# Kernel optimization log

Hardware: AMD Instinct MI355X
Metric: run time of the kernel (lower is better)

## Reference

```python
import jax, jax.numpy as jnp
import numpy as np

M_POOL = 12500  # rows of the down_transform sparse matrix


def setup_inputs() -> dict:
    key = jax.random.key(0)
    ks = jax.random.split(key, 6)
    B, N, E, Cin, Cout, K, P = 4, 50000, 800000, 32, 64, 6, 50000
    x = jax.random.normal(ks[0], (B, N, Cin), jnp.float32)
    edge_index = jax.random.randint(ks[1], (2, E), 0, N, dtype=jnp.int64)
    pool_row = jax.random.randint(ks[2], (P,), 0, M_POOL, dtype=jnp.int64)
    pool_col = jax.random.randint(ks[3], (P,), 0, N, dtype=jnp.int64)
    pool_val = jax.random.uniform(ks[4], (P,), jnp.float32)
    # xavier_uniform over each [Cin, Cout] slice; bias zero-init (reset_parameters)
    limit = np.sqrt(6.0 / (Cin + Cout)).astype(np.float32)
    weight = jax.random.uniform(ks[5], (K, Cin, Cout), jnp.float32, -limit, limit)
    bias = jnp.zeros((Cout,), jnp.float32)
    return dict(x=x, edge_index=edge_index, pool_row=pool_row,
                pool_col=pool_col, pool_val=pool_val, weight=weight, bias=bias)


def _cheb_conv(x, edge_index, weight, bias):
    # x: [B, N, Cin]; weight: [K, Cin, Cout]
    N = x.shape[1]
    row, col = edge_index[0], edge_index[1]
    ones = jnp.ones(row.shape, x.dtype)
    deg = jax.ops.segment_sum(ones, row, num_segments=N)
    dis = jnp.where(deg > 0, jax.lax.rsqrt(jnp.where(deg > 0, deg, 1.0)), 0.0)
    # L_hat = 2L/lambda_max - I with lambda_max=2, sym norm -> diag 0, off-diag -d_i^-1/2 d_j^-1/2
    norm = -dis[row] * dis[col]  # [E]

    def prop(h):  # h: [B, N, C] -> L_hat @ h (gather, scale, scatter_add)
        msgs = h[:, col, :] * norm[None, :, None]  # [B, E, C]
        return jnp.zeros_like(h).at[:, row, :].add(msgs)

    Tx0 = x
    out = jnp.einsum('bnc,co->bno', Tx0, weight[0])
    Tx1 = prop(Tx0)
    out = out + jnp.einsum('bnc,co->bno', Tx1, weight[1])
    for k in range(2, weight.shape[0]):
        Tx2 = 2.0 * prop(Tx1) - Tx0
        out = out + jnp.einsum('bnc,co->bno', Tx2, weight[k])
        Tx0, Tx1 = Tx1, Tx2
    return out + bias


def reference(x, edge_index, pool_row, pool_col, pool_val, weight, bias):
    h = _cheb_conv(x, edge_index, weight, bias)  # single block (n_blocks=1)
    h = jax.nn.elu(h)
    # Pool: gather columns, scale by sparse values, scatter_add into rows
    B, _, C = h.shape
    gathered = h[:, pool_col, :] * pool_val[None, :, None]  # [B, P, C]
    out = jnp.zeros((B, M_POOL, C), h.dtype).at[:, pool_row, :].add(gathered)
    return out
```

## Files before the change

### kernel.cpp

```cpp
#include <hip/hip_runtime.h>
#include <hip/hip_fp16.h>
#include <cstdint>

#define N_NODES 50000
#define B_SZ 4
#define C_IN 32
#define C_OUT 64
#define K_CHEB 6
#define M_POOL 12500
#define NT_ROWS (N_NODES + M_POOL)
#define NS32 ((size_t)N_NODES * C_IN)
#define ZH ((size_t)N_NODES * C_OUT)
#define CN_CAP 2048
#define DSTR 16

typedef _Float16 f16x8 __attribute__((ext_vector_type(8)));
typedef float f32x4 __attribute__((ext_vector_type(4)));
typedef unsigned short ushort_t;

__device__ __forceinline__ unsigned short f2h(float f) {
    union { _Float16 h; unsigned short u; } v;
    v.h = (_Float16)f;
    return v.u;
}

__device__ __forceinline__ float h2f(unsigned short u) {
    union { unsigned short u; _Float16 h; } v;
    v.u = u;
    return (float)v.h;
}

__device__ __forceinline__ __half2 u2h2(unsigned u) { return __builtin_bit_cast(__half2, u); }
__device__ __forceinline__ unsigned h22u(__half2 h) { return __builtin_bit_cast(unsigned, h); }

__global__ void zero_deg_kernel(int* __restrict__ deg_s) {
    int i = blockIdx.x * 256 + threadIdx.x;
    if (i < NT_ROWS * DSTR) deg_s[i] = 0;
}

__global__ void deg_slot_kernel(const int* __restrict__ row, const int* __restrict__ prow,
                                int* __restrict__ deg_s, int* __restrict__ slot, int E, int P) {
    int e = blockIdx.x * blockDim.x + threadIdx.x;
    if (e < E) slot[e] = atomicAdd(&deg_s[row[e] * DSTR], 1);
    else if (e < E + P) slot[e] = atomicAdd(&deg_s[(N_NODES + prow[e - E]) * DSTR], 1);
}

__global__ void disdegp_kernel(const int* __restrict__ deg_s, float* __restrict__ dis,
                               int* __restrict__ degp) {
    int i = blockIdx.x * blockDim.x + threadIdx.x;
    if (i < N_NODES) {
        int d = deg_s[i * DSTR];
        dis[i] = d > 0 ? rsqrtf((float)d) : 0.f;
        degp[i] = (d + 7) & ~7;
    } else if (i < NT_ROWS) {
        degp[i] = deg_s[i * DSTR];
    }
}

__global__ void block_sum_kernel(const int* __restrict__ degp, int* __restrict__ bsum, int N) {
    __shared__ int sm[256];
    int i = blockIdx.x * 256 + threadIdx.x;
    sm[threadIdx.x] = (i < N) ? degp[i] : 0;
    __syncthreads();
    for (int s = 128; s > 0; s >>= 1) {
        if (threadIdx.x < s) sm[threadIdx.x] += sm[threadIdx.x + s];
        __syncthreads();
    }
    if (threadIdx.x == 0) bsum[blockIdx.x] = sm[0];
}

__global__ void scan_bsum_kernel(int* bsum, int nb, int* rowptr, int N) {
    __shared__ int sm[256];
    int t = threadIdx.x;
    int v = (t < nb) ? bsum[t] : 0;
    sm[t] = v;
    __syncthreads();
    for (int off = 1; off < 256; off <<= 1) {
        int u = (t >= off) ? sm[t - off] : 0;
        __syncthreads();
        sm[t] += u;
        __syncthreads();
    }
    if (t < nb) bsum[t] = sm[t] - v;
    if (t == 0) rowptr[N] = sm[255];
}

__global__ void rowptr_kernel(const int* __restrict__ degp, const int* __restrict__ bsum,
                              int* __restrict__ rowptr, int N) {
    __shared__ int sm[256];
    int i = blockIdx.x * 256 + threadIdx.x;
    sm[threadIdx.x] = (i < N) ? degp[i] : 0;
    __syncthreads();
    if (threadIdx.x == 0) {
        int run = bsum[blockIdx.x];
        for (int t = 0; t < 256; t++) { int v = sm[t]; sm[t] = run; run += v; }
    }
    __syncthreads();
    if (i < N) rowptr[i] = sm[threadIdx.x];
}

__global__ void pad_fill_kernel(const int* __restrict__ deg_s, const int* __restrict__ rowptr,
                                int2* __restrict__ cn) {
    int r = blockIdx.x * blockDim.x + threadIdx.x;
    if (r >= N_NODES) return;
    int p = rowptr[r] + deg_s[r * DSTR];
    int p1 = rowptr[r + 1];
    for (; p < p1; ++p) cn[p] = make_int2(0, 0);
}

__global__ void place_all_kernel(const int* __restrict__ row, const int* __restrict__ col,
                                 const int* __restrict__ prow, const int* __restrict__ pcol,
                                 const float* __restrict__ pval, const float* __restrict__ dis,
                                 const int* __restrict__ rowptr, const int* __restrict__ slot,
                                 int2* __restrict__ cn, int E, int P) {
    int e = blockIdx.x * blockDim.x + threadIdx.x;
    if (e < E) {
        int r = row[e], c = col[e];
        float nm = -dis[r] * dis[c];
        unsigned h = f2h(nm);
        cn[rowptr[r] + slot[e]] = make_int2(c, (int)(h | (h << 16)));
    } else if (e < E + P) {
        int i = e - E;
        int r = N_NODES + prow[i];
        cn[rowptr[r] + slot[e]] = make_int2(pcol[i], __float_as_int(pval[i]));
    }
}

__global__ void cast_h_kernel(const float* __restrict__ in, unsigned int* __restrict__ out,
                              int n2) {
    int i = blockIdx.x * 256 + threadIdx.x;
    if (i < n2) {
        unsigned a = f2h(in[2 * i]), b = f2h(in[2 * i + 1]);
        out[i] = a | (b << 16);
    }
}

__global__ void __launch_bounds__(256, 8)
prop_kernel(const ushort_t* __restrict__ hf, const ushort_t* __restrict__ p2f,
            ushort_t* __restrict__ outf,
            const int* __restrict__ rowptr, const int2* __restrict__ cn, float alpha) {
    __shared__ int2 lcn[CN_CAP];
    int bid = blockIdx.x;
    int b = bid & 3;
    int grp = bid >> 2;
    int r0 = grp * 64;
    int rend = r0 + 64 > N_NODES ? N_NODES : r0 + 64;
    int pbase = rowptr[r0];
    int pend = rowptr[rend];
    int cnt = pend - pbase;
    bool use_lds = (cnt <= CN_CAP);
    if (use_lds) {
        for (int i = threadIdx.x; i < cnt; i += 256) lcn[i] = cn[pbase + i];
    }
    __syncthreads();

    int lr = threadIdx.x >> 2;
    int cs = threadIdx.x & 3;
    int r = r0 + lr;
    if (r >= N_NODES) return;
    const char* hb = (const char*)hf + (size_t)b * NS32 * 2;
    unsigned coff = (unsigned)cs * 16u;
    __half2 a0 = __float2half2_rn(0.f), a1 = a0, a2 = a0, a3 = a0;

    if (use_lds) {
        int p0 = rowptr[r] - pbase, p1 = rowptr[r + 1] - pbase;
        for (int p = p0; p < p1; p += 8) {
            unsigned off[8];
            __half2 n[8];
#pragma unroll
            for (int i = 0; i < 8; i++) {
                int2 e = lcn[p + i];
                off[i] = ((unsigned)e.x << 6) + coff;
                n[i] = u2h2((unsigned)e.y);
            }
            uint4 v[8];
#pragma unroll
            for (int i = 0; i < 8; i++) v[i] = *(const uint4*)(hb + off[i]);
#pragma unroll
            for (int i = 0; i < 8; i++) {
                a0 = __hfma2(u2h2(v[i].x), n[i], a0);
                a1 = __hfma2(u2h2(v[i].y), n[i], a1);
                a2 = __hfma2(u2h2(v[i].z), n[i], a2);
                a3 = __hfma2(u2h2(v[i].w), n[i], a3);
            }
        }
    } else {
        int p0 = rowptr[r], p1 = rowptr[r + 1];
        for (int p = p0; p < p1; p += 8) {
            unsigned off[8];
            __half2 n[8];
#pragma unroll
            for (int i = 0; i < 8; i++) {
                int2 e = cn[p + i];
                off[i] = ((unsigned)e.x << 6) + coff;
                n[i] = u2h2((unsigned)e.y);
            }
            uint4 v[8];
#pragma unroll
            for (int i = 0; i < 8; i++) v[i] = *(const uint4*)(hb + off[i]);
#pragma unroll
            for (int i = 0; i < 8; i++) {
                a0 = __hfma2(u2h2(v[i].x), n[i], a0);
                a1 = __hfma2(u2h2(v[i].y), n[i], a1);
                a2 = __hfma2(u2h2(v[i].z), n[i], a2);
                a3 = __hfma2(u2h2(v[i].w), n[i], a3);
            }
        }
    }

    unsigned ooff = ((unsigned)r << 6) + coff;
    uint4 o;
    if (p2f) {
        __half2 al2 = __float2half2_rn(alpha);
        uint4 pv = *(const uint4*)((const char*)p2f + (size_t)b * NS32 * 2 + ooff);
        o.x = h22u(__hfma2(a0, al2, __hneg2(u2h2(pv.x))));
        o.y = h22u(__hfma2(a1, al2, __hneg2(u2h2(pv.y))));
        o.z = h22u(__hfma2(a2, al2, __hneg2(u2h2(pv.z))));
        o.w = h22u(__hfma2(a3, al2, __hneg2(u2h2(pv.w))));
    } else {
        o.x = h22u(a0); o.y = h22u(a1); o.z = h22u(a2); o.w = h22u(a3);
    }
    *(uint4*)((char*)outf + (size_t)b * NS32 * 2 + ooff) = o;
}

__global__ void packW_kernel(const float* __restrict__ W, ushort_t* __restrict__ Wp) {
    int i = blockIdx.x * 256 + threadIdx.x;
    if (i >= K_CHEB * 4 * 64 * 8) return;
    int j = i & 7;
    int lane = (i >> 3) & 63;
    int t = (i >> 9) & 3;
    int s = i >> 11;
    int k = (lane >> 4) * 8 + j;
    int col = t * 16 + (lane & 15);
    Wp[i] = f2h(W[((size_t)s * C_IN + k) * C_OUT + col]);
}

__global__ void gemm_mfma_kernel(const ushort_t* __restrict__ T0, const ushort_t* __restrict__ T1,
                                 const ushort_t* __restrict__ T2, const ushort_t* __restrict__ T3,
                                 const ushort_t* __restrict__ T4, const ushort_t* __restrict__ T5,
                                 const ushort_t* __restrict__ Wp,
                                 const float* __restrict__ bias, ushort_t* __restrict__ z) {
    int lane = threadIdx.x & 63;
    int wave = (blockIdx.x << 2) + (threadIdx.x >> 6);
    int r0 = wave << 4;
    int ga = r0 + (lane & 15);
    int koff = (lane >> 4) * 8;
    const ushort_t* Ts[6] = {T0, T1, T2, T3, T4, T5};

    f16x8 afr[6];
#pragma unroll
    for (int s = 0; s < 6; s++)
        afr[s] = *(const f16x8*)(Ts[s] + (size_t)ga * C_IN + koff);

    int orow = r0 + ((lane >> 4) << 2);
#pragma unroll
    for (int t = 0; t < 4; t++) {
        f32x4 acc = {0.f, 0.f, 0.f, 0.f};
#pragma unroll
        for (int s = 0; s < 6; s++) {
            f16x8 bfr = *(const f16x8*)(Wp + ((s * 4 + t) * 64 + lane) * 8);
            acc = __builtin_amdgcn_mfma_f32_16x16x32_f16(afr[s], bfr, acc, 0, 0, 0);
        }
        int col = (t << 4) + (lane & 15);
        float bv = bias[col];
#pragma unroll
        for (int rg = 0; rg < 4; rg++) {
            float v = acc[rg] + bv;
            z[(size_t)(orow + rg) * C_OUT + col] = f2h(v > 0.f ? v : (expf(v) - 1.f));
        }
    }
}

__global__ void pool_csr_kernel(const ushort_t* __restrict__ z, const int* __restrict__ rowptr,
                                const int2* __restrict__ cn, float* __restrict__ out) {
    int bid = blockIdx.x;
    int b = bid & 3;
    int r = (bid >> 2) * 8 + (threadIdx.x >> 5);
    int c2 = threadIdx.x & 31;
    if (r >= M_POOL) return;
    const char* zb = (const char*)z + (size_t)b * ZH * 2;
    unsigned coff = (unsigned)c2 << 2;
    float s0 = 0.f, s1 = 0.f;
    int p0 = rowptr[N_NODES + r], p1 = rowptr[N_NODES + r + 1];
    for (int p = p0; p < p1; ++p) {
        int2 e = cn[p];
        float v = __int_as_float(e.y);
        unsigned u = *(const unsigned*)(zb + (((unsigned)e.x << 7) + coff));
        s0 += h2f((ushort_t)u) * v;
        s1 += h2f((ushort_t)(u >> 16)) * v;
    }
    size_t idx = (size_t)b * M_POOL * C_OUT + (size_t)r * C_OUT + 2 * c2;
    *(float2*)&out[idx] = make_float2(s0, s1);
}

extern "C" void kernel_launch(void* const* d_in, const int* in_sizes, int n_in,
                              void* d_out, int out_size, void* d_ws, size_t ws_size,
                              hipStream_t stream) {
    const float* x    = (const float*)d_in[0];
    const int*   ei   = (const int*)d_in[1];
    const int*   prow = (const int*)d_in[2];
    const int*   pcol = (const int*)d_in[3];
    const float* pval = (const float*)d_in[4];
    const float* W    = (const float*)d_in[5];
    const float* bias = (const float*)d_in[6];
    const int E = in_sizes[1] / 2;
    const int P = in_sizes[2];
    const int* row = ei;
    const int* col = ei + E;
    const int EP_MAX = E + 7 * N_NODES + P;

    char* ws = (char*)d_ws;
    size_t o = 0;
    auto alloc = [&](size_t bytes) -> char* {
        char* p = ws + o;
        o += (bytes + 255) & ~(size_t)255;
        return p;
    };
    int nb = (NT_ROWS + 255) / 256;
    int*   deg_s  = (int*)alloc((size_t)NT_ROWS * DSTR * 4);
    int*   degp   = (int*)alloc((size_t)NT_ROWS * 4);
    float* dis    = (float*)alloc((size_t)N_NODES * 4);
    int*   rowptr = (int*)alloc((size_t)(NT_ROWS + 1) * 4);
    int*   slot   = (int*)alloc((size_t)(E + P) * 4);
    int*   bsum   = (int*)alloc((size_t)nb * 4);
    int2*  cn     = (int2*)alloc((size_t)EP_MAX * 8);
    ushort_t* Wp  = (ushort_t*)alloc((size_t)K_CHEB * 4 * 64 * 8 * 2);
    ushort_t* xh  = (ushort_t*)alloc((size_t)B_SZ * NS32 * 2);
    ushort_t* hA  = (ushort_t*)alloc((size_t)B_SZ * NS32 * 2);
    ushort_t* hB  = (ushort_t*)alloc((size_t)B_SZ * NS32 * 2);
    ushort_t* hC  = (ushort_t*)alloc((size_t)B_SZ * NS32 * 2);
    ushort_t* hD  = (ushort_t*)alloc((size_t)B_SZ * NS32 * 2);
    ushort_t* hE  = (ushort_t*)alloc((size_t)B_SZ * NS32 * 2);
    ushort_t* z   = (ushort_t*)alloc((size_t)B_SZ * ZH * 2);

    zero_deg_kernel<<<(NT_ROWS * DSTR + 255) / 256, 256, 0, stream>>>(deg_s);
    deg_slot_kernel<<<(E + P + 255) / 256, 256, 0, stream>>>(row, prow, deg_s, slot, E, P);
    disdegp_kernel<<<nb, 256, 0, stream>>>(deg_s, dis, degp);
    block_sum_kernel<<<nb, 256, 0, stream>>>(degp, bsum, NT_ROWS);
    scan_bsum_kernel<<<1, 256, 0, stream>>>(bsum, nb, rowptr, NT_ROWS);
    rowptr_kernel<<<nb, 256, 0, stream>>>(degp, bsum, rowptr, NT_ROWS);
    pad_fill_kernel<<<(N_NODES + 255) / 256, 256, 0, stream>>>(deg_s, rowptr, cn);
    place_all_kernel<<<(E + P + 255) / 256, 256, 0, stream>>>(row, col, prow, pcol, pval, dis,
                                                              rowptr, slot, cn, E, P);
    packW_kernel<<<(K_CHEB * 4 * 64 * 8 + 255) / 256, 256, 0, stream>>>(W, Wp);
    int n2 = (int)(B_SZ * NS32 / 2);
    cast_h_kernel<<<(n2 + 255) / 256, 256, 0, stream>>>(x, (unsigned int*)xh, n2);

    int prop_blocks = ((N_NODES + 63) / 64) * B_SZ;
    int gemm_blocks = (B_SZ * N_NODES) / 64;

    prop_kernel<<<prop_blocks, 256, 0, stream>>>(xh, nullptr, hA, rowptr, cn, 1.0f);
    prop_kernel<<<prop_blocks, 256, 0, stream>>>(hA, xh, hB, rowptr, cn, 2.0f);
    prop_kernel<<<prop_blocks, 256, 0, stream>>>(hB, hA, hC, rowptr, cn, 2.0f);
    prop_kernel<<<prop_blocks, 256, 0, stream>>>(hC, hB, hD, rowptr, cn, 2.0f);
    prop_kernel<<<prop_blocks, 256, 0, stream>>>(hD, hC, hE, rowptr, cn, 2.0f);
    gemm_mfma_kernel<<<gemm_blocks, 256, 0, stream>>>(xh, hA, hB, hC, hD, hE, Wp, bias, z);
    pool_csr_kernel<<<((M_POOL + 7) / 8) * B_SZ, 256, 0, stream>>>(z, rowptr, cn,
                                                                   (float*)d_out);
}
```

Before: 253.6 us.

## Fuse setup kernels, parallelize rowptr scan, add nontemporal loads/stores

```diff
diff --git a/kernel.cpp b/kernel.cpp
--- a/kernel.cpp
+++ b/kernel.cpp
@@ -13,9 +13,11 @@
 #define ZH ((size_t)N_NODES * C_OUT)
 #define CN_CAP 2048
 #define DSTR 16
+#define NWELEM (K_CHEB * 4 * 64 * 8)
 
 typedef _Float16 f16x8 __attribute__((ext_vector_type(8)));
 typedef float f32x4 __attribute__((ext_vector_type(4)));
+typedef unsigned int u32x4 __attribute__((ext_vector_type(4)));
 typedef unsigned short ushort_t;
 
 __device__ __forceinline__ unsigned short f2h(float f) {
@@ -45,22 +47,21 @@
     else if (e < E + P) slot[e] = atomicAdd(&deg_s[(N_NODES + prow[e - E]) * DSTR], 1);
 }
 
-__global__ void disdegp_kernel(const int* __restrict__ deg_s, float* __restrict__ dis,
-                               int* __restrict__ degp) {
-    int i = blockIdx.x * blockDim.x + threadIdx.x;
+__global__ void disdegp_bsum_kernel(const int* __restrict__ deg_s, float* __restrict__ dis,
+                                    int* __restrict__ degp, int* __restrict__ bsum) {
+    __shared__ int sm[256];
+    int i = blockIdx.x * 256 + threadIdx.x;
+    int dp = 0;
     if (i < N_NODES) {
         int d = deg_s[i * DSTR];
         dis[i] = d > 0 ? rsqrtf((float)d) : 0.f;
-        degp[i] = (d + 7) & ~7;
+        dp = (d + 7) & ~7;
+        degp[i] = dp;
     } else if (i < NT_ROWS) {
-        degp[i] = deg_s[i * DSTR];
-    }
-}
-
-__global__ void block_sum_kernel(const int* __restrict__ degp, int* __restrict__ bsum, int N) {
-    __shared__ int sm[256];
-    int i = blockIdx.x * 256 + threadIdx.x;
-    sm[threadIdx.x] = (i < N) ? degp[i] : 0;
+        dp = deg_s[i * DSTR];
+        degp[i] = dp;
+    }
+    sm[threadIdx.x] = dp;
     __syncthreads();
     for (int s = 128; s > 0; s >>= 1) {
         if (threadIdx.x < s) sm[threadIdx.x] += sm[threadIdx.x + s];
@@ -89,29 +90,24 @@
                               int* __restrict__ rowptr, int N) {
     __shared__ int sm[256];
     int i = blockIdx.x * 256 + threadIdx.x;
-    sm[threadIdx.x] = (i < N) ? degp[i] : 0;
+    int t = threadIdx.x;
+    int v = (i < N) ? degp[i] : 0;
+    sm[t] = v;
     __syncthreads();
-    if (threadIdx.x == 0) {
-        int run = bsum[blockIdx.x];
-        for (int t = 0; t < 256; t++) { int v = sm[t]; sm[t] = run; run += v; }
-    }
-    __syncthreads();
-    if (i < N) rowptr[i] = sm[threadIdx.x];
-}
-
-__global__ void pad_fill_kernel(const int* __restrict__ deg_s, const int* __restrict__ rowptr,
-                                int2* __restrict__ cn) {
-    int r = blockIdx.x * blockDim.x + threadIdx.x;
-    if (r >= N_NODES) return;
-    int p = rowptr[r] + deg_s[r * DSTR];
-    int p1 = rowptr[r + 1];
-    for (; p < p1; ++p) cn[p] = make_int2(0, 0);
-}
-
-__global__ void place_all_kernel(const int* __restrict__ row, const int* __restrict__ col,
+    for (int off = 1; off < 256; off <<= 1) {
+        int u = (t >= off) ? sm[t - off] : 0;
+        __syncthreads();
+        sm[t] += u;
+        __syncthreads();
+    }
+    if (i < N) rowptr[i] = bsum[blockIdx.x] + sm[t] - v;
+}
+
+__global__ void place_pad_kernel(const int* __restrict__ row, const int* __restrict__ col,
                                  const int* __restrict__ prow, const int* __restrict__ pcol,
                                  const float* __restrict__ pval, const float* __restrict__ dis,
                                  const int* __restrict__ rowptr, const int* __restrict__ slot,
+                                 const int* __restrict__ deg_s,
                                  int2* __restrict__ cn, int E, int P) {
     int e = blockIdx.x * blockDim.x + threadIdx.x;
     if (e < E) {
@@ -123,15 +119,32 @@
         int i = e - E;
         int r = N_NODES + prow[i];
         cn[rowptr[r] + slot[e]] = make_int2(pcol[i], __float_as_int(pval[i]));
-    }
-}
-
-__global__ void cast_h_kernel(const float* __restrict__ in, unsigned int* __restrict__ out,
-                              int n2) {
+    } else if (e < E + P + N_NODES) {
+        int r = e - E - P;
+        int p = rowptr[r] + deg_s[r * DSTR];
+        int p1 = rowptr[r + 1];
+        for (; p < p1; ++p) cn[p] = make_int2(0, 0);
+    }
+}
+
+__global__ void packW_cast_kernel(const float* __restrict__ W, ushort_t* __restrict__ Wp,
+                                  const float* __restrict__ xin, unsigned int* __restrict__ xout,
+                                  int n2) {
     int i = blockIdx.x * 256 + threadIdx.x;
-    if (i < n2) {
-        unsigned a = f2h(in[2 * i]), b = f2h(in[2 * i + 1]);
-        out[i] = a | (b << 16);
+    if (i < NWELEM) {
+        int j = i & 7;
+        int lane = (i >> 3) & 63;
+        int t = (i >> 9) & 3;
+        int s = i >> 11;
+        int k = (lane >> 4) * 8 + j;
+        int colw = t * 16 + (lane & 15);
+        Wp[i] = f2h(W[((size_t)s * C_IN + k) * C_OUT + colw]);
+    } else {
+        int c = i - NWELEM;
+        if (c < n2) {
+            unsigned a = f2h(xin[2 * c]), b = f2h(xin[2 * c + 1]);
+            xout[c] = a | (b << 16);
+        }
     }
 }
 
@@ -150,7 +163,11 @@
     int cnt = pend - pbase;
     bool use_lds = (cnt <= CN_CAP);
     if (use_lds) {
-        for (int i = threadIdx.x; i < cnt; i += 256) lcn[i] = cn[pbase + i];
+        for (int i = threadIdx.x; i < cnt; i += 256) {
+            unsigned long long u =
+                __builtin_nontemporal_load((const unsigned long long*)(cn + pbase + i));
+            lcn[i] = make_int2((int)(unsigned)(u & 0xffffffffULL), (int)(unsigned)(u >> 32));
+        }
     }
     __syncthreads();
 
@@ -209,30 +226,19 @@
     }
 
     unsigned ooff = ((unsigned)r << 6) + coff;
-    uint4 o;
+    u32x4 o;
     if (p2f) {
         __half2 al2 = __float2half2_rn(alpha);
-        uint4 pv = *(const uint4*)((const char*)p2f + (size_t)b * NS32 * 2 + ooff);
-        o.x = h22u(__hfma2(a0, al2, __hneg2(u2h2(pv.x))));
-        o.y = h22u(__hfma2(a1, al2, __hneg2(u2h2(pv.y))));
-        o.z = h22u(__hfma2(a2, al2, __hneg2(u2h2(pv.z))));
-        o.w = h22u(__hfma2(a3, al2, __hneg2(u2h2(pv.w))));
+        u32x4 pv = __builtin_nontemporal_load(
+            (const u32x4*)((const char*)p2f + (size_t)b * NS32 * 2 + ooff));
+        o[0] = h22u(__hfma2(a0, al2, __hneg2(u2h2(pv[0]))));
+        o[1] = h22u(__hfma2(a1, al2, __hneg2(u2h2(pv[1]))));
+        o[2] = h22u(__hfma2(a2, al2, __hneg2(u2h2(pv[2]))));
+        o[3] = h22u(__hfma2(a3, al2, __hneg2(u2h2(pv[3]))));
     } else {
-        o.x = h22u(a0); o.y = h22u(a1); o.z = h22u(a2); o.w = h22u(a3);
-    }
-    *(uint4*)((char*)outf + (size_t)b * NS32 * 2 + ooff) = o;
-}
-
-__global__ void packW_kernel(const float* __restrict__ W, ushort_t* __restrict__ Wp) {
-    int i = blockIdx.x * 256 + threadIdx.x;
-    if (i >= K_CHEB * 4 * 64 * 8) return;
-    int j = i & 7;
-    int lane = (i >> 3) & 63;
-    int t = (i >> 9) & 3;
-    int s = i >> 11;
-    int k = (lane >> 4) * 8 + j;
-    int col = t * 16 + (lane & 15);
-    Wp[i] = f2h(W[((size_t)s * C_IN + k) * C_OUT + col]);
+        o[0] = h22u(a0); o[1] = h22u(a1); o[2] = h22u(a2); o[3] = h22u(a3);
+    }
+    __builtin_nontemporal_store(o, (u32x4*)((char*)outf + (size_t)b * NS32 * 2 + ooff));
 }
 
 __global__ void gemm_mfma_kernel(const ushort_t* __restrict__ T0, const ushort_t* __restrict__ T1,
@@ -283,9 +289,11 @@
     float s0 = 0.f, s1 = 0.f;
     int p0 = rowptr[N_NODES + r], p1 = rowptr[N_NODES + r + 1];
     for (int p = p0; p < p1; ++p) {
-        int2 e = cn[p];
-        float v = __int_as_float(e.y);
-        unsigned u = *(const unsigned*)(zb + (((unsigned)e.x << 7) + coff));
+        unsigned long long eu =
+            __builtin_nontemporal_load((const unsigned long long*)(cn + p));
+        unsigned ex = (unsigned)(eu & 0xffffffffULL);
+        float v = __uint_as_float((unsigned)(eu >> 32));
+        unsigned u = *(const unsigned*)(zb + ((ex << 7) + coff));
         s0 += h2f((ushort_t)u) * v;
         s1 += h2f((ushort_t)(u >> 16)) * v;
     }
@@ -324,7 +332,7 @@
     int*   slot   = (int*)alloc((size_t)(E + P) * 4);
     int*   bsum   = (int*)alloc((size_t)nb * 4);
     int2*  cn     = (int2*)alloc((size_t)EP_MAX * 8);
-    ushort_t* Wp  = (ushort_t*)alloc((size_t)K_CHEB * 4 * 64 * 8 * 2);
+    ushort_t* Wp  = (ushort_t*)alloc((size_t)NWELEM * 2);
     ushort_t* xh  = (ushort_t*)alloc((size_t)B_SZ * NS32 * 2);
     ushort_t* hA  = (ushort_t*)alloc((size_t)B_SZ * NS32 * 2);
     ushort_t* hB  = (ushort_t*)alloc((size_t)B_SZ * NS32 * 2);
@@ -335,16 +343,14 @@
 
     zero_deg_kernel<<<(NT_ROWS * DSTR + 255) / 256, 256, 0, stream>>>(deg_s);
     deg_slot_kernel<<<(E + P + 255) / 256, 256, 0, stream>>>(row, prow, deg_s, slot, E, P);
-    disdegp_kernel<<<nb, 256, 0, stream>>>(deg_s, dis, degp);
-    block_sum_kernel<<<nb, 256, 0, stream>>>(degp, bsum, NT_ROWS);
+    disdegp_bsum_kernel<<<nb, 256, 0, stream>>>(deg_s, dis, degp, bsum);
     scan_bsum_kernel<<<1, 256, 0, stream>>>(bsum, nb, rowptr, NT_ROWS);
     rowptr_kernel<<<nb, 256, 0, stream>>>(degp, bsum, rowptr, NT_ROWS);
-    pad_fill_kernel<<<(N_NODES + 255) / 256, 256, 0, stream>>>(deg_s, rowptr, cn);
-    place_all_kernel<<<(E + P + 255) / 256, 256, 0, stream>>>(row, col, prow, pcol, pval, dis,
-                                                              rowptr, slot, cn, E, P);
-    packW_kernel<<<(K_CHEB * 4 * 64 * 8 + 255) / 256, 256, 0, stream>>>(W, Wp);
+    place_pad_kernel<<<(E + P + N_NODES + 255) / 256, 256, 0, stream>>>(
+        row, col, prow, pcol, pval, dis, rowptr, slot, deg_s, cn, E, P);
     int n2 = (int)(B_SZ * NS32 / 2);
-    cast_h_kernel<<<(n2 + 255) / 256, 256, 0, stream>>>(x, (unsigned int*)xh, n2);
+    packW_cast_kernel<<<(NWELEM + n2 + 255) / 256, 256, 0, stream>>>(W, Wp, x,
+                                                                     (unsigned int*)xh, n2);
 
     int prop_blocks = ((N_NODES + 63) / 64) * B_SZ;
     int gemm_blocks = (B_SZ * N_NODES) / 64;
```

After: 269.0 us. 1.06x slower.
